# Kernel optimization log

Hardware: AMD Instinct MI355X
Metric: run time of the kernel (lower is better)

## Reference

```python
import jax, jax.numpy as jnp
import numpy as np
import math

MID = 48       # mid_channels
HEADS = 4      # num_heads
POS = 16       # mid_channels // 3 (row/col positional channels)


def _unfold(x, p):
    """nn.Unfold with kernel p, padding p//2: (..., H, W) -> (..., p, p, H, W)."""
    H, W = x.shape[-2], x.shape[-1]
    pad = p // 2
    xp = jnp.pad(x, [(0, 0)] * (x.ndim - 2) + [(pad, pad), (pad, pad)])
    return jnp.stack(
        [jnp.stack([xp[..., k:k + H, l:l + W] for l in range(p)], axis=-3)
         for k in range(p)], axis=-4)


def _pe_mlp(idx, w1, b1, g, b, w2, b2):
    """Conv2d(1->16,1x1) -> LayerNorm(16) -> Swish -> Conv2d(16->POS,1x1) on scalar coords."""
    t = idx.reshape(-1, 1)                         # (N,1)
    h = t @ w1.T + b1                              # (N,16)
    mu = jnp.mean(h, -1, keepdims=True)
    var = jnp.var(h, -1, keepdims=True)
    h = (h - mu) * jax.lax.rsqrt(var + 1e-5) * g + b
    h = h * jax.nn.sigmoid(h)                      # Swish
    e = h @ w2.T + b2                              # (N,POS)
    return e.reshape(idx.shape + (e.shape[-1],))   # (V,P,P,POS)


def setup_inputs() -> dict:
    key = jax.random.key(0)
    ks = jax.random.split(key, 32)
    B, Cin, G, H, W, P, Cout = 2, 32, 4, 28, 28, 7, 64

    def n(k, shp, s=0.05):
        return jax.random.normal(k, shp, dtype=jnp.float32) * s

    inp = {"x": jax.random.normal(ks[0], (B, Cin, G, H, W), dtype=jnp.float32)}
    inp["Wq"] = n(ks[1], (MID * HEADS, Cin)); inp["bq"] = n(ks[2], (MID * HEADS,))
    inp["Wk"] = n(ks[3], (MID * HEADS, Cin)); inp["bk"] = n(ks[4], (MID * HEADS,))
    inp["Wv"] = n(ks[5], (MID * HEADS, Cin)); inp["bv"] = n(ks[6], (MID * HEADS,))
    inp["Wout"] = n(ks[7], (Cout, MID * HEADS)); inp["bout"] = n(ks[8], (Cout,))
    inp["row_w1"] = n(ks[9], (16, 1)); inp["row_b1"] = n(ks[10], (16,))
    inp["row_ln_g"] = jnp.ones((16,), jnp.float32); inp["row_ln_b"] = jnp.zeros((16,), jnp.float32)
    inp["row_w2"] = n(ks[11], (POS, 16)); inp["row_b2"] = n(ks[12], (POS,))
    inp["col_w1"] = n(ks[13], (16, 1)); inp["col_b1"] = n(ks[14], (16,))
    inp["col_ln_g"] = jnp.ones((16,), jnp.float32); inp["col_ln_b"] = jnp.zeros((16,), jnp.float32)
    inp["col_w2"] = n(ks[15], (POS, 16)); inp["col_b2"] = n(ks[16], (POS,))
    inp["group_emb"] = n(ks[17], (G, MID - 2 * POS))
    # rotated relative spatial positions, normalized to [-1, 1]
    lin = np.linspace(-1.0, 1.0, P).astype(np.float32)
    r = np.repeat(lin[:, None], P, 1)
    c = np.repeat(lin[None, :], P, 0)
    rows, cols = [], []
    for v in range(G):
        th = v * math.pi / 2.0
        rows.append(math.cos(th) * r - math.sin(th) * c)
        cols.append(math.sin(th) * r + math.cos(th) * c)
    inp["row_indices"] = jnp.asarray(np.stack(rows, 0))
    inp["col_indices"] = jnp.asarray(np.stack(cols, 0))
    # acted relative group positions for cyclic group C4
    ar = np.arange(G)
    gi = (ar[:, None, None] + ar[None, None, :] - ar[None, :, None]) % G
    inp["g_indices"] = jnp.asarray(gi, dtype=jnp.int32)
    return inp


def _forward(x, Wq, bq, Wk, bk, Wv, bv, Wout, bout,
             row_w1, row_b1, row_ln_g, row_ln_b, row_w2, row_b2,
             col_w1, col_b1, col_ln_g, col_ln_b, col_w2, col_b2,
             group_emb, row_indices, col_indices, g_indices):
    B, Cin, G, H, W = x.shape
    P = row_indices.shape[-1]
    sqn = jnp.sqrt(jnp.float32(Cin))

    def proj(Wm, bm):  # 1x1 Conv3d -> (B, MID, HEADS, G, H, W)
        y = jnp.einsum('oi,bigyx->bogyx', Wm, x) + bm[None, :, None, None, None]
        return y.reshape(B, MID, HEADS, G, H, W)

    q = proj(Wq, bq)
    k = proj(Wk, bk)
    v = proj(Wv, bv)
    k_loc = _unfold(k, P)   # (B, MID, HEADS, G, P, P, H, W)
    v_loc = _unfold(v, P)

    content = jnp.einsum('bchgij,bchmklij->bhgijmkl', q, k_loc)
    row_e = _pe_mlp(row_indices, row_w1, row_b1, row_ln_g, row_ln_b, row_w2, row_b2)
    col_e = _pe_mlp(col_indices, col_w1, col_b1, col_ln_g, col_ln_b, col_w2, col_b2)
    row_s = jnp.einsum('bchgij,vklc->bhvgijkl', q[:, :POS], row_e)
    col_s = jnp.einsum('bchgij,vklc->bhvgijkl', q[:, POS:2 * POS], col_e)
    g_e = group_emb[g_indices]                              # (V, G, M, gdim)
    g_s = jnp.einsum('bchgij,vgmc->bhvgijm', q[:, 2 * POS:], g_e)

    # scores: (b, h, v, g, i, j, m, k, l)
    scores = (row_s[:, :, :, :, :, :, None] + col_s[:, :, :, :, :, :, None]
              + g_s[..., None, None] + content[:, :, None]) / sqn

    # mask patch positions that fall outside the image (-inf -> prob 0)
    valid = _unfold(jnp.ones((H, W), jnp.float32), P)       # (P, P, H, W)
    valid = jnp.transpose(valid, (2, 3, 0, 1))[None, None, None, None, :, :, None, :, :]
    scores = jnp.where(valid > 0.5, scores, -jnp.inf)

    shp = scores.shape
    probs = jax.nn.softmax(scores.reshape(shp[:-3] + (-1,)), axis=-1).reshape(shp)

    o = jnp.einsum('bhvgijmkl,bchmklij->bchvij', probs, v_loc)  # (B, MID, HEADS, V, H, W)
    o = o.reshape(B, MID * HEADS, G, H, W)
    return jnp.einsum('oi,bivyx->bovyx', Wout, o) + bout[None, :, None, None, None]


def reference(x, Wq, bq, Wk, bk, Wv, bv, Wout, bout,
              row_w1, row_b1, row_ln_g, row_ln_b, row_w2, row_b2,
              col_w1, col_b1, col_ln_g, col_ln_b, col_w2, col_b2,
              group_emb, row_indices, col_indices, g_indices):
    return _forward(x, Wq, bq, Wk, bk, Wv, bv, Wout, bout,
                    row_w1, row_b1, row_ln_g, row_ln_b, row_w2, row_b2,
                    col_w1, col_b1, col_ln_g, col_ln_b, col_w2, col_b2,
                    group_emb, row_indices, col_indices, g_indices)
```

## Files before the change

### kernel.cpp

```cpp
#include <hip/hip_runtime.h>
#include <math.h>

#define Bb   2
#define CIN  32
#define Gg   4
#define NH   4
#define Hh   28
#define Ww   28
#define HW   784
#define Pp   7
#define PP   49
#define MID  48
#define COUT 64
#define OC   192

#define QOFF  0
#define KOFF  1204224
#define VOFF  2408448
#define OOFF  3612672

#define KSCALE 0.2550611135387359f

__device__ unsigned g_peT2[Gg * PP * 16];
__device__ unsigned g_geT2[8 * 64];
__device__ float    g_WT2[OC * COUT];

typedef _Float16 h2f __attribute__((ext_vector_type(2)));

__device__ __forceinline__ unsigned packh2(float a, float b) {
    auto r = __builtin_amdgcn_cvt_pkrtz(a, b);
    return __builtin_bit_cast(unsigned, r);
}

__device__ __forceinline__ float fdot2(unsigned a, unsigned b, float c) {
    return __builtin_amdgcn_fdot2(__builtin_bit_cast(h2f, a),
                                  __builtin_bit_cast(h2f, b), c, false);
}

__device__ __forceinline__ float exp2_fast(float x) {
    float r;
    asm("v_exp_f32 %0, %1" : "=v"(r) : "v"(x));
    return r;
}

__global__ __launch_bounds__(192) void qkvpe_kernel(const float* __restrict__ x,
    const float* __restrict__ Wq, const float* __restrict__ bq,
    const float* __restrict__ Wk, const float* __restrict__ bk,
    const float* __restrict__ Wv, const float* __restrict__ bv,
    const float* row_w1, const float* row_b1,
    const float* row_g,  const float* row_bb,
    const float* row_w2, const float* row_b2,
    const float* col_w1, const float* col_b1,
    const float* col_g,  const float* col_bb,
    const float* col_w2, const float* col_b2,
    const float* row_idx, const float* col_idx,
    const float* group_emb, const int* g_indices,
    const float* Wout,
    float* __restrict__ ws)
{
    __shared__ float xs[CIN * 16];
    __shared__ float wtmp[16 * 193];
    int tid = threadIdx.x;
    if (blockIdx.x == Bb * Gg * Hh * 2) {
        for (int t = tid; t < 2 * Gg * PP; t += 192) {
            int half = t / (Gg * PP);
            int n    = t - half * (Gg * PP);
            int v = n / PP, kl = n % PP;
            const float* w1 = half ? col_w1 : row_w1;
            const float* b1 = half ? col_b1 : row_b1;
            const float* lg = half ? col_g  : row_g;
            const float* lb = half ? col_bb : row_bb;
            const float* w2 = half ? col_w2 : row_w2;
            const float* b2 = half ? col_b2 : row_b2;
            float tv = half ? col_idx[n] : row_idx[n];

            float hb[16];
            float mean = 0.f;
            for (int k = 0; k < 16; k++) { hb[k] = tv * w1[k] + b1[k]; mean += hb[k]; }
            mean *= (1.f / 16.f);
            float var = 0.f;
            for (int k = 0; k < 16; k++) { float d = hb[k] - mean; var += d * d; }
            var *= (1.f / 16.f);
            float inv = 1.f / sqrtf(var + 1e-5f);
            for (int k = 0; k < 16; k++) {
                float hn = (hb[k] - mean) * inv * lg[k] + lb[k];
                hb[k] = hn / (1.f + expf(-hn));
            }
            float accv[16];
            for (int p = 0; p < 16; p++) {
                float acc = b2[p];
                for (int k = 0; k < 16; k++) acc += hb[k] * w2[p * 16 + k];
                accv[p] = acc * KSCALE;
            }
            for (int i2 = 0; i2 < 8; i2++)
                g_peT2[(v * PP + kl) * 16 + half * 8 + i2] =
                    packh2(accv[2 * i2], accv[2 * i2 + 1]);
        }
        for (int t = tid; t < 64; t += 192) {
            int gi = g_indices[t];
            for (int i2 = 0; i2 < 8; i2++)
                g_geT2[i2 * 64 + t] = packh2(group_emb[gi * 16 + 2 * i2] * KSCALE,
                                             group_emb[gi * 16 + 2 * i2 + 1] * KSCALE);
        }
        for (int chunk = 0; chunk < 4; chunk++) {
            int obase = chunk * 16;
            __syncthreads();
            for (int idx = tid; idx < 16 * OC; idx += 192) {
                int ol = idx / OC, t = idx % OC;
                wtmp[ol * 193 + t] = Wout[(obase + ol) * OC + t];
            }
            __syncthreads();
            for (int idx = tid; idx < 16 * OC; idx += 192) {
                int tp = idx / 16, ol = idx % 16;
                int h = tp / MID, c = tp % MID;
                g_WT2[tp * 64 + obase + ol] = wtmp[ol * 193 + c * NH + h];
            }
        }
        return;
    }

    int r = blockIdx.x;
    int jh = r & 1; r >>= 1;
    int i = r % Hh; r /= Hh;
    int g = r & 3;  int b = r >> 2;
    int j0 = jh * 14;

    for (int idx = tid; idx < CIN * 14; idx += 192) {
        int ci = idx / 14, jj = idx % 14;
        xs[ci * 16 + jj] = x[((b * CIN + ci) * Gg + g) * HW + i * Ww + j0 + jj];
    }
    __syncthreads();

    int h = tid / MID, c = tid % MID;
    int oo = c * NH + h;
    int wbase = (((b * NH + h) * Gg + g) * HW + i * Ww + j0) * MID + c;

    const float* Wm[3]  = {Wq, Wk, Wv};
    const float* bm[3]  = {bq, bk, bv};
    const int    off[3] = {QOFF, KOFF, VOFF};
    const float  scl[3] = {1.0f, KSCALE, 1.0f};
    for (int p = 0; p < 3; p++) {
        const float4* Wr4 = (const float4*)(Wm[p] + oo * CIN);
        float bias = bm[p][oo];
        float a[14];
        #pragma unroll
        for (int j = 0; j < 14; j++) a[j] = bias;

        #pragma unroll 2
        for (int ci8 = 0; ci8 < 8; ci8++) {
            float4 wv4 = Wr4[ci8];
            int cb = ci8 * 4;
#define CHAN(WV, CI)                                                          \
            {                                                                 \
                float wv = WV;                                                \
                float4 xA = *(const float4*)&xs[(CI) * 16 + 0];               \
                float4 xB = *(const float4*)&xs[(CI) * 16 + 4];               \
                float4 xC = *(const float4*)&xs[(CI) * 16 + 8];               \
                float2 xD = *(const float2*)&xs[(CI) * 16 + 12];              \
                a[0] += wv * xA.x;  a[1] += wv * xA.y;                        \
                a[2] += wv * xA.z;  a[3] += wv * xA.w;                        \
                a[4] += wv * xB.x;  a[5] += wv * xB.y;                        \
                a[6] += wv * xB.z;  a[7] += wv * xB.w;                        \
                a[8] += wv * xC.x;  a[9] += wv * xC.y;                        \
                a[10] += wv * xC.z; a[11] += wv * xC.w;                       \
                a[12] += wv * xD.x; a[13] += wv * xD.y;                       \
            }
            CHAN(wv4.x, cb + 0)
            CHAN(wv4.y, cb + 1)
            CHAN(wv4.z, cb + 2)
            CHAN(wv4.w, cb + 3)
#undef CHAN
        }
        float s = scl[p];
        #pragma unroll
        for (int j = 0; j < 14; j++) ws[off[p] + wbase + j * MID] = a[j] * s;
    }
}

__global__ __launch_bounds__(256, 4) void attn_kernel(float* __restrict__ ws)
{
    __shared__ __align__(16) unsigned kvb[7560];
    __shared__ __align__(16) unsigned pp2[4][PP][8];
    __shared__ __align__(16) unsigned qp[4][4][32];
    __shared__ __align__(16) float gsm[4][64];

    const int tid  = threadIdx.x;
    const int wave = tid >> 6;
    const int lane = tid & 63;

    int blk = blockIdx.x;
    int j0 = (blk % 7) * 4;
    int i  = (blk / 7) % Hh;
    int bh = blk / (7 * Hh);
    int b = bh >> 2, h = bh & 3;
    int j  = j0 + wave;
    int ij = i * Ww + j;

    const float* Qt  = ws + QOFF;
    const float* Kbh = ws + KOFF + (size_t)bh * Gg * HW * MID;
    const float* Vbh = ws + VOFF + (size_t)bh * Gg * HW * MID;
    float* Ot = ws + OOFF;

    if (lane < 48) {
        int g = lane / 12, c4 = lane % 12;
        float4 qv = *(const float4*)&Qt[((size_t)(bh * Gg + g) * HW + ij) * MID + c4 * 4];
        qp[wave][g][c4 * 2]     = packh2(qv.x, qv.y);
        qp[wave][g][c4 * 2 + 1] = packh2(qv.z, qv.w);
    }

    #pragma unroll
    for (int s = 0; s < 4; s++) {
        int t = tid + s * 256;
        if (t < 840) {
            int c4 = t % 12, cl = t / 12;
            int gy = i - 3 + cl / 10, gx = j0 - 3 + cl % 10;
            bool ok = ((unsigned)gy < Hh) && ((unsigned)gx < Ww);
            const float* kp = &Kbh[(size_t)(gy * Ww + gx) * MID + c4 * 4];
            #pragma unroll
            for (int m = 0; m < 4; m++) {
                float4 val = {0.f, 0.f, 0.f, 0.f};
                if (ok) val = *(const float4*)(kp + (size_t)m * HW * MID);
                *(uint2*)&kvb[(m * 70 + cl) * 27 + c4 * 2] =
                    make_uint2(packh2(val.x, val.y), packh2(val.z, val.w));
            }
        }
    }

    int kk = lane / Pp, ll = lane % Pp;
    int cell = (lane < PP) ? kk * 10 + ll + wave : 0;
    bool vmask = (lane < PP) && ((unsigned)(i + kk - 3) < Hh) && ((unsigned)(j + ll - 3) < Ww);
    int lclamp = lane < PP ? lane : 0;

    float per[4][4] = {};
    #pragma unroll
    for (int u4 = 0; u4 < 4; u4++) {
        uint4 qA = *(const uint4*)&qp[wave][0][u4 * 4];
        uint4 qB = *(const uint4*)&qp[wave][1][u4 * 4];
        uint4 qC = *(const uint4*)&qp[wave][2][u4 * 4];
        uint4 qD = *(const uint4*)&qp[wave][3][u4 * 4];
        #pragma unroll
        for (int v = 0; v < 4; v++) {
            uint4 pk = *(const uint4*)&g_peT2[(v * PP + lclamp) * 16 + u4 * 4];
            per[v][0] = fdot2(pk.w, qA.w, fdot2(pk.z, qA.z, fdot2(pk.y, qA.y, fdot2(pk.x, qA.x, per[v][0]))));
            per[v][1] = fdot2(pk.w, qB.w, fdot2(pk.z, qB.z, fdot2(pk.y, qB.y, fdot2(pk.x, qB.x, per[v][1]))));
            per[v][2] = fdot2(pk.w, qC.w, fdot2(pk.z, qC.z, fdot2(pk.y, qC.y, fdot2(pk.x, qC.x, per[v][2]))));
            per[v][3] = fdot2(pk.w, qD.w, fdot2(pk.z, qD.z, fdot2(pk.y, qD.y, fdot2(pk.x, qD.x, per[v][3]))));
        }
    }
    if (!vmask) {
        #pragma unroll
        for (int v = 0; v < 4; v++)
            #pragma unroll
            for (int g = 0; g < 4; g++) per[v][g] = -INFINITY;
    }

    {
        int g = (lane >> 2) & 3;
        float ga = 0.f;
        #pragma unroll
        for (int u = 0; u < 8; u++)
            ga = fdot2(g_geT2[u * 64 + lane], qp[wave][g][16 + u], ga);
        gsm[wave][lane] = ga;
    }
    __syncthreads();

    float acc[4][4] = {};
    #pragma unroll 2
    for (int u4 = 0; u4 < 6; u4++) {
        uint4 qA = *(const uint4*)&qp[wave][0][u4 * 4];
        uint4 qB = *(const uint4*)&qp[wave][1][u4 * 4];
        uint4 qC = *(const uint4*)&qp[wave][2][u4 * 4];
        uint4 qD = *(const uint4*)&qp[wave][3][u4 * 4];
        #pragma unroll
        for (int m = 0; m < 4; m++) {
            int base = (m * 70 + cell) * 27 + u4 * 4;
            uint2 k01 = *(const uint2*)&kvb[base];
            uint2 k23 = *(const uint2*)&kvb[base + 2];
            acc[m][0] = fdot2(k23.y, qA.w, fdot2(k23.x, qA.z, fdot2(k01.y, qA.y, fdot2(k01.x, qA.x, acc[m][0]))));
            acc[m][1] = fdot2(k23.y, qB.w, fdot2(k23.x, qB.z, fdot2(k01.y, qB.y, fdot2(k01.x, qB.x, acc[m][1]))));
            acc[m][2] = fdot2(k23.y, qC.w, fdot2(k23.x, qC.z, fdot2(k01.y, qC.y, fdot2(k01.x, qC.x, acc[m][2]))));
            acc[m][3] = fdot2(k23.y, qD.w, fdot2(k23.x, qD.z, fdot2(k01.y, qD.y, fdot2(k01.x, qD.x, acc[m][3]))));
        }
    }

    float ppr[4][4] = {};
    #pragma unroll
    for (int v = 0; v < 4; v++) {
        #pragma unroll
        for (int g = 0; g < 4; g++) {
            int vg = v * 4 + g;
            float4 gs = *(const float4*)&gsm[wave][vg * 4];
            float ex[4];
            ex[0] = exp2_fast(acc[0][g] + per[v][g] + gs.x);
            ex[1] = exp2_fast(acc[1][g] + per[v][g] + gs.y);
            ex[2] = exp2_fast(acc[2][g] + per[v][g] + gs.z);
            ex[3] = exp2_fast(acc[3][g] + per[v][g] + gs.w);
            float ls = ex[0] + ex[1] + ex[2] + ex[3];
            #pragma unroll
            for (int d = 32; d > 0; d >>= 1) ls += __shfl_xor(ls, d, 64);
            float rinv = 1.0f / ls;
            #pragma unroll
            for (int m = 0; m < 4; m++) ppr[v][m] += ex[m] * rinv;
        }
    }
    if (lane < PP) {
        uint4 w0, w1;
        w0.x = packh2(ppr[0][0], ppr[0][1]); w0.y = packh2(ppr[0][2], ppr[0][3]);
        w0.z = packh2(ppr[1][0], ppr[1][1]); w0.w = packh2(ppr[1][2], ppr[1][3]);
        w1.x = packh2(ppr[2][0], ppr[2][1]); w1.y = packh2(ppr[2][2], ppr[2][3]);
        w1.z = packh2(ppr[3][0], ppr[3][1]); w1.w = packh2(ppr[3][2], ppr[3][3]);
        *(uint4*)&pp2[wave][lane][0] = w0;
        *(uint4*)&pp2[wave][lane][4] = w1;
    }
    __syncthreads();

    for (int t = tid; t < 840; t += 256) {
        int c4 = t % 12; int cl = t / 12;
        int gy = i - 3 + cl / 10, gx = j0 - 3 + cl % 10;
        float4 v0 = {0.f,0.f,0.f,0.f}, v1 = v0, v2 = v0, v3 = v0;
        if ((unsigned)gy < Hh && (unsigned)gx < Ww) {
            const float* vp = &Vbh[((size_t)(gy * Ww + gx)) * MID + c4 * 4];
            v0 = *(const float4*)vp;
            v1 = *(const float4*)(vp + (size_t)HW * MID);
            v2 = *(const float4*)(vp + (size_t)2 * HW * MID);
            v3 = *(const float4*)(vp + (size_t)3 * HW * MID);
        }
        uint4 wA, wB;
        wA.x = packh2(v0.x, v1.x); wA.y = packh2(v2.x, v3.x);
        wA.z = packh2(v0.y, v1.y); wA.w = packh2(v2.y, v3.y);
        wB.x = packh2(v0.z, v1.z); wB.y = packh2(v2.z, v3.z);
        wB.z = packh2(v0.w, v1.w); wB.w = packh2(v2.w, v3.w);
        *(uint4*)&kvb[(cl * 48 + c4 * 4) * 2    ] = wA;
        *(uint4*)&kvb[(cl * 48 + c4 * 4) * 2 + 4] = wB;
    }
    __syncthreads();

    if (lane < MID) {
        float o0 = 0.f, o1 = 0.f, o2 = 0.f, o3 = 0.f;
        const uint4* ppw = (const uint4*)&pp2[wave][0][0];
        for (int kk2 = 0; kk2 < Pp; kk2++) {
            #pragma unroll
            for (int ll2 = 0; ll2 < Pp; ll2++) {
                int kl2  = kk2 * Pp + ll2;
                int cell2 = kk2 * 10 + ll2 + wave;
                uint2 vv = *(const uint2*)&kvb[(cell2 * 48 + lane) * 2];
                uint4 A = ppw[kl2 * 2];
                uint4 B = ppw[kl2 * 2 + 1];
                o0 = fdot2(vv.y, A.y, fdot2(vv.x, A.x, o0));
                o1 = fdot2(vv.y, A.w, fdot2(vv.x, A.z, o1));
                o2 = fdot2(vv.y, B.y, fdot2(vv.x, B.x, o2));
                o3 = fdot2(vv.y, B.w, fdot2(vv.x, B.z, o3));
            }
        }
        Ot[((size_t)(b * Gg + 0) * HW + ij) * OC + h * MID + lane] = o0;
        Ot[((size_t)(b * Gg + 1) * HW + ij) * OC + h * MID + lane] = o1;
        Ot[((size_t)(b * Gg + 2) * HW + ij) * OC + h * MID + lane] = o2;
        Ot[((size_t)(b * Gg + 3) * HW + ij) * OC + h * MID + lane] = o3;
    }
}

__global__ __launch_bounds__(256) void outproj_kernel(const float* __restrict__ bout,
                                                      const float* __restrict__ ws,
                                                      float* __restrict__ out)
{
    __shared__ float ov[16 * 193];
    __shared__ float res[64 * 17];
    int tid = threadIdx.x;
    int p0 = blockIdx.x * 16;
    const float* Ot = ws + OOFF;

    for (int idx = tid; idx < 16 * OC; idx += 256) {
        int pl = idx / OC, t = idx % OC;
        ov[pl * 193 + t] = Ot[(size_t)(p0 + pl) * OC + t];
    }
    __syncthreads();

    int o = tid & 63, pg = tid >> 6;
    float a0 = bout[o], a1 = a0, a2 = a0, a3 = a0;
    for (int t = 0; t < OC; t++) {
        float w = g_WT2[t * 64 + o];
        a0 += w * ov[(pg     ) * 193 + t];
        a1 += w * ov[(pg +  4) * 193 + t];
        a2 += w * ov[(pg +  8) * 193 + t];
        a3 += w * ov[(pg + 12) * 193 + t];
    }
    res[o * 17 + pg     ] = a0;
    res[o * 17 + pg +  4] = a1;
    res[o * 17 + pg +  8] = a2;
    res[o * 17 + pg + 12] = a3;
    __syncthreads();

    for (int idx = tid; idx < 1024; idx += 256) {
        int o2 = idx >> 4, pl = idx & 15;
        int p = p0 + pl;
        int ij2 = p % HW; int bv = p / HW; int v = bv & 3; int bb = bv >> 2;
        out[((bb * COUT + o2) * Gg + v) * HW + ij2] = res[o2 * 17 + pl];
    }
}

extern "C" void kernel_launch(void* const* d_in, const int* in_sizes, int n_in,
                              void* d_out, int out_size, void* d_ws, size_t ws_size,
                              hipStream_t stream)
{
    const float* x      = (const float*)d_in[0];
    const float* Wq     = (const float*)d_in[1];
    const float* bq     = (const float*)d_in[2];
    const float* Wk     = (const float*)d_in[3];
    const float* bk     = (const float*)d_in[4];
    const float* Wv     = (const float*)d_in[5];
    const float* bv     = (const float*)d_in[6];
    const float* Wout   = (const float*)d_in[7];
    const float* bout   = (const float*)d_in[8];
    const float* row_w1 = (const float*)d_in[9];
    const float* row_b1 = (const float*)d_in[10];
    const float* row_g  = (const float*)d_in[11];
    const float* row_bb = (const float*)d_in[12];
    const float* row_w2 = (const float*)d_in[13];
    const float* row_b2 = (const float*)d_in[14];
    const float* col_w1 = (const float*)d_in[15];
    const float* col_b1 = (const float*)d_in[16];
    const float* col_g  = (const float*)d_in[17];
    const float* col_bb = (const float*)d_in[18];
    const float* col_w2 = (const float*)d_in[19];
    const float* col_b2 = (const float*)d_in[20];
    const float* gemb   = (const float*)d_in[21];
    const float* ridx   = (const float*)d_in[22];
    const float* cidx   = (const float*)d_in[23];
    const int*   gidx   = (const int*)d_in[24];

    float* ws  = (float*)d_ws;
    float* out = (float*)d_out;

    qkvpe_kernel<<<Bb * Gg * Hh * 2 + 1, 192, 0, stream>>>(
        x, Wq, bq, Wk, bk, Wv, bv,
        row_w1, row_b1, row_g, row_bb, row_w2, row_b2,
        col_w1, col_b1, col_g, col_bb, col_w2, col_b2,
        ridx, cidx, gemb, gidx, Wout, ws);
    attn_kernel<<<Bb * NH * Hh * (Ww / 4), 256, 0, stream>>>(ws);
    outproj_kernel<<<Bb * Gg * HW / 16, 256, 0, stream>>>(bout, ws, out);
}
```

Baseline: 176.0 us.

## Prefetch V tile into registers before softmax, split V LDS planes, remap blocks

The V-tile global loads are issued into registers before the softmax phase, so their latency overlaps the exp/shuffle work instead of stalling after the barrier. The leftover 72 elements are loaded after the barrier. The V LDS layout is split into two planes (v0/v1 pairs and v2/v3 pairs), so the PV loop reads single 32-bit words with a fully unrolled 49-step loop. Block indices are also permuted across 8 strides, likely to spread blocks over XCDs or L2. The prefetch costs about 48 extra VGPRs per thread, which may lower occupancy under launch_bounds(256,4).

```diff
diff --git a/kernel.cpp b/kernel.cpp
--- a/kernel.cpp
+++ b/kernel.cpp
@@ -20,6 +20,8 @@
 #define OOFF  3612672
 
 #define KSCALE 0.2550611135387359f
+
+#define VP1F 3360
 
 __device__ unsigned g_peT2[Gg * PP * 16];
 __device__ unsigned g_geT2[8 * 64];
@@ -188,7 +190,7 @@
     const int wave = tid >> 6;
     const int lane = tid & 63;
 
-    int blk = blockIdx.x;
+    int blk = (blockIdx.x & 7) * 196 + (blockIdx.x >> 3);
     int j0 = (blk % 7) * 4;
     int i  = (blk / 7) % Hh;
     int bh = blk / (7 * Hh);
@@ -283,6 +285,22 @@
         }
     }
 
+    float4 pv[3][4];
+    #pragma unroll
+    for (int s = 0; s < 3; s++) {
+        int t = tid + s * 256;
+        int c4 = t % 12, cl = t / 12;
+        int gy = i - 3 + cl / 10, gx = j0 - 3 + cl % 10;
+        #pragma unroll
+        for (int m = 0; m < 4; m++) pv[s][m] = make_float4(0.f, 0.f, 0.f, 0.f);
+        if ((unsigned)gy < Hh && (unsigned)gx < Ww) {
+            const float* vp = &Vbh[((size_t)(gy * Ww + gx)) * MID + c4 * 4];
+            #pragma unroll
+            for (int m = 0; m < 4; m++)
+                pv[s][m] = *(const float4*)(vp + (size_t)m * HW * MID);
+        }
+    }
+
     float ppr[4][4] = {};
     #pragma unroll
     for (int v = 0; v < 4; v++) {
@@ -314,43 +332,61 @@
     }
     __syncthreads();
 
-    for (int t = tid; t < 840; t += 256) {
-        int c4 = t % 12; int cl = t / 12;
+    float4 q30 = {0.f,0.f,0.f,0.f}, q31 = q30, q32 = q30, q33 = q30;
+    if (tid < 72) {
+        int t = tid + 768;
+        int c4 = t % 12, cl = t / 12;
         int gy = i - 3 + cl / 10, gx = j0 - 3 + cl % 10;
-        float4 v0 = {0.f,0.f,0.f,0.f}, v1 = v0, v2 = v0, v3 = v0;
         if ((unsigned)gy < Hh && (unsigned)gx < Ww) {
             const float* vp = &Vbh[((size_t)(gy * Ww + gx)) * MID + c4 * 4];
-            v0 = *(const float4*)vp;
-            v1 = *(const float4*)(vp + (size_t)HW * MID);
-            v2 = *(const float4*)(vp + (size_t)2 * HW * MID);
-            v3 = *(const float4*)(vp + (size_t)3 * HW * MID);
-        }
+            q30 = *(const float4*)vp;
+            q31 = *(const float4*)(vp + (size_t)HW * MID);
+            q32 = *(const float4*)(vp + (size_t)2 * HW * MID);
+            q33 = *(const float4*)(vp + (size_t)3 * HW * MID);
+        }
+    }
+    #pragma unroll
+    for (int s = 0; s < 3; s++) {
+        int t = tid + s * 256;
+        int c4 = t % 12, cl = t / 12;
+        float4 v0 = pv[s][0], v1 = pv[s][1], v2 = pv[s][2], v3 = pv[s][3];
         uint4 wA, wB;
-        wA.x = packh2(v0.x, v1.x); wA.y = packh2(v2.x, v3.x);
-        wA.z = packh2(v0.y, v1.y); wA.w = packh2(v2.y, v3.y);
-        wB.x = packh2(v0.z, v1.z); wB.y = packh2(v2.z, v3.z);
-        wB.z = packh2(v0.w, v1.w); wB.w = packh2(v2.w, v3.w);
-        *(uint4*)&kvb[(cl * 48 + c4 * 4) * 2    ] = wA;
-        *(uint4*)&kvb[(cl * 48 + c4 * 4) * 2 + 4] = wB;
+        wA.x = packh2(v0.x, v1.x); wA.y = packh2(v0.y, v1.y);
+        wA.z = packh2(v0.z, v1.z); wA.w = packh2(v0.w, v1.w);
+        wB.x = packh2(v2.x, v3.x); wB.y = packh2(v2.y, v3.y);
+        wB.z = packh2(v2.z, v3.z); wB.w = packh2(v2.w, v3.w);
+        *(uint4*)&kvb[cl * 48 + c4 * 4] = wA;
+        *(uint4*)&kvb[VP1F + cl * 48 + c4 * 4] = wB;
+    }
+    if (tid < 72) {
+        int t = tid + 768;
+        int c4 = t % 12, cl = t / 12;
+        uint4 wA, wB;
+        wA.x = packh2(q30.x, q31.x); wA.y = packh2(q30.y, q31.y);
+        wA.z = packh2(q30.z, q31.z); wA.w = packh2(q30.w, q31.w);
+        wB.x = packh2(q32.x, q33.x); wB.y = packh2(q32.y, q33.y);
+        wB.z = packh2(q32.z, q33.z); wB.w = packh2(q32.w, q33.w);
+        *(uint4*)&kvb[cl * 48 + c4 * 4] = wA;
+        *(uint4*)&kvb[VP1F + cl * 48 + c4 * 4] = wB;
     }
     __syncthreads();
 
     if (lane < MID) {
         float o0 = 0.f, o1 = 0.f, o2 = 0.f, o3 = 0.f;
         const uint4* ppw = (const uint4*)&pp2[wave][0][0];
-        for (int kk2 = 0; kk2 < Pp; kk2++) {
-            #pragma unroll
-            for (int ll2 = 0; ll2 < Pp; ll2++) {
-                int kl2  = kk2 * Pp + ll2;
-                int cell2 = kk2 * 10 + ll2 + wave;
-                uint2 vv = *(const uint2*)&kvb[(cell2 * 48 + lane) * 2];
-                uint4 A = ppw[kl2 * 2];
-                uint4 B = ppw[kl2 * 2 + 1];
-                o0 = fdot2(vv.y, A.y, fdot2(vv.x, A.x, o0));
-                o1 = fdot2(vv.y, A.w, fdot2(vv.x, A.z, o1));
-                o2 = fdot2(vv.y, B.y, fdot2(vv.x, B.x, o2));
-                o3 = fdot2(vv.y, B.w, fdot2(vv.x, B.z, o3));
-            }
+        const unsigned* v0b = &kvb[wave * 48 + lane];
+        const unsigned* v1b = v0b + VP1F;
+        #pragma unroll
+        for (int kl2 = 0; kl2 < PP; kl2++) {
+            int cellc = (kl2 / Pp) * 10 + (kl2 % Pp);
+            unsigned vv0 = v0b[cellc * 48];
+            unsigned vv1 = v1b[cellc * 48];
+            uint4 A = ppw[kl2 * 2];
+            uint4 B = ppw[kl2 * 2 + 1];
+            o0 = fdot2(vv1, A.y, fdot2(vv0, A.x, o0));
+            o1 = fdot2(vv1, A.w, fdot2(vv0, A.z, o1));
+            o2 = fdot2(vv1, B.y, fdot2(vv0, B.x, o2));
+            o3 = fdot2(vv1, B.w, fdot2(vv0, B.z, o3));
         }
         Ot[((size_t)(b * Gg + 0) * HW + ij) * OC + h * MID + lane] = o0;
         Ot[((size_t)(b * Gg + 1) * HW + ij) * OC + h * MID + lane] = o1;
```

After: 187.2 us. +6.4%, slower.
